# Performance work log

Measured on AMD Instinct MI355X. Metric: run time of the kernel, lower is better.

## Reference

```python
import jax, jax.numpy as jnp
import numpy as np

B, T_IN, T_OUT, V, C = 2048, 10, 25, 22, 3
D = V * C            # embed / gru hidden = 66
H = 3                # attention heads
HD = D // H          # head dim = 22
EPS = 1e-5
DIMS = [(C, 64), (64, 32), (32, 64), (64, C)]


def _bn(x, g, b):
    # eval-mode BatchNorm2d with default running stats (mean=0, var=1)
    return x * (g / jnp.sqrt(1.0 + EPS))[None, :, None, None] + b[None, :, None, None]


def _gcn_layer(x, A, Tm, cw, cb, g, bt, rw, rb, rg, rbt, pre):
    # x: (N, Cin, T, V); STSGCN ST_GCNN_layer with 1x1 conv (kernel [1,1])
    res = _bn(jnp.einsum('nctv,oc->notv', x, rw) + rb[None, :, None, None], rg, rbt)
    y = jnp.einsum('nctv,vtq->ncqv', x, Tm)   # temporal mixing
    y = jnp.einsum('nctv,tvw->nctw', y, A)    # spatial (joint) mixing
    y = _bn(jnp.einsum('nctv,oc->notv', y, cw) + cb[None, :, None, None], g, bt)
    y = y + res
    return jnp.where(y >= 0, y, pre * y)      # PReLU (scalar slope)


def setup_inputs() -> dict:
    key = jax.random.key(0)
    ks = iter(jax.random.split(key, 64))
    def rn(shape, s=0.05):
        return jax.random.normal(next(ks), shape, dtype=jnp.float32) * s
    d = {"x": rn((B, T_IN, V, C), 1.0)}
    d["A"] = rn((4, T_IN, V, V), 0.2)
    d["Tm"] = rn((4, V, T_IN, T_IN), 0.3)
    d["pre"] = jnp.full((4,), 0.25, jnp.float32)
    for i, (ci, co) in enumerate(DIMS):
        d[f"cw{i}"] = rn((co, ci), 0.1)
        d[f"cb{i}"] = rn((co,), 0.1)
        d[f"g{i}"] = jnp.ones((co,), jnp.float32)
        d[f"bt{i}"] = jnp.zeros((co,), jnp.float32)
        d[f"rw{i}"] = rn((co, ci), 0.1)
        d[f"rb{i}"] = rn((co,), 0.1)
        d[f"rg{i}"] = jnp.ones((co,), jnp.float32)
        d[f"rbt{i}"] = jnp.zeros((co,), jnp.float32)
    d["gru_wi"] = rn((3 * D, D)); d["gru_wh"] = rn((3 * D, D))
    d["gru_bi"] = rn((3 * D,));   d["gru_bh"] = rn((3 * D,))
    d["qkv_w"] = rn((3 * D, D)); d["qkv_b"] = rn((3 * D,))
    d["ow"] = rn((D, D)); d["ob"] = rn((D,))
    d["lw"] = rn((D, 2 * D)); d["lb"] = rn((D,))
    return d


def _forward(x, A, Tm, pre, cws, cbs, gs, bts, rws, rbs, rgs, rbts,
             gru_wi, gru_wh, gru_bi, gru_bh, qkv_w, qkv_b, ow, ob, lw, lb):
    raw = x.reshape(B, T_IN, D)                 # (N,T,V*C), joint-major flatten
    h = jnp.transpose(x, (0, 3, 1, 2))          # (N,C,T,V)
    for i in range(4):
        h = _gcn_layer(h, A[i], Tm[i], cws[i], cbs[i], gs[i], bts[i],
                       rws[i], rbs[i], rgs[i], rbts[i], pre[i])
    enc = jnp.transpose(h, (0, 2, 3, 1)).reshape(B, T_IN, D)  # (N,T,V*C)

    wq, wk, wv = qkv_w[:D], qkv_w[D:2 * D], qkv_w[2 * D:]
    bq, bk, bv = qkv_b[:D], qkv_b[D:2 * D], qkv_b[2 * D:]
    # K,V of encoder sequence are constant across decode steps: project once
    k = (enc @ wk.T + bk).reshape(B, T_IN, H, HD)
    v = (enc @ wv.T + bv).reshape(B, T_IN, H, HD)
    scale = 1.0 / jnp.sqrt(jnp.float32(HD))

    def gru(inp, hprev):
        gi = inp @ gru_wi.T + gru_bi
        gh = hprev @ gru_wh.T + gru_bh
        ir, iz, inn = jnp.split(gi, 3, axis=-1)
        hr, hz, hn = jnp.split(gh, 3, axis=-1)
        r = jax.nn.sigmoid(ir + hr)
        z = jax.nn.sigmoid(iz + hz)
        n = jnp.tanh(inn + r * hn)
        return (1.0 - z) * n + z * hprev

    def step(carry, _):
        hs, tp = carry
        hs = gru(tp, hs)
        q = ((hs @ wq.T + bq) * scale).reshape(B, H, HD)
        scores = jnp.einsum('bhd,bthd->bht', q, k)
        attn = jax.nn.softmax(scores, axis=-1)
        ctx = jnp.einsum('bht,bthd->bhd', attn, v).reshape(B, D) @ ow.T + ob
        pred = jnp.concatenate([hs, ctx], axis=-1) @ lw.T + lb + tp  # residual
        return (hs, pred), pred

    h0 = enc[:, -1, :]
    tp0 = raw[:, -1, :]
    _, preds = jax.lax.scan(step, (h0, tp0), None, length=T_OUT)
    out = jnp.transpose(preds, (1, 0, 2))       # (N, T_out, D)
    return out.reshape(B, T_OUT, V, C)


def reference(x, A, Tm, pre,
              cw0, cb0, g0, bt0, rw0, rb0, rg0, rbt0,
              cw1, cb1, g1, bt1, rw1, rb1, rg1, rbt1,
              cw2, cb2, g2, bt2, rw2, rb2, rg2, rbt2,
              cw3, cb3, g3, bt3, rw3, rb3, rg3, rbt3,
              gru_wi, gru_wh, gru_bi, gru_bh, qkv_w, qkv_b, ow, ob, lw, lb):
    return _forward(x, A, Tm, pre,
                    [cw0, cw1, cw2, cw3], [cb0, cb1, cb2, cb3],
                    [g0, g1, g2, g3], [bt0, bt1, bt2, bt3],
                    [rw0, rw1, rw2, rw3], [rb0, rb1, rb2, rb3],
                    [rg0, rg1, rg2, rg3], [rbt0, rbt1, rbt2, rbt3],
                    gru_wi, gru_wh, gru_bi, gru_bh, qkv_w, qkv_b, ow, ob, lw, lb)
```

## Files before the change

### kernel.cpp

```cpp
#include <hip/hip_runtime.h>

#define DEV static __device__ __forceinline__


struct EncW {
  const float* cw[4]; const float* cb[4]; const float* g[4]; const float* bt[4];
  const float* rw[4]; const float* rb[4]; const float* rg[4]; const float* rbt[4];
};

template<int CI, int CO>
DEV void gcn_layer32(int tid,
    const float* __restrict__ cw, const float* __restrict__ cb,
    const float* __restrict__ gg, const float* __restrict__ bt,
    const float* __restrict__ rw, const float* __restrict__ rb,
    const float* __restrict__ rg, const float* __restrict__ rbt,
    const float* __restrict__ TmL, const float* __restrict__ AL, float preL,
    float* __restrict__ act, float* __restrict__ S,
    float* __restrict__ rmul, float* __restrict__ radd,
    float* __restrict__ cmul, float* __restrict__ cadd)
{
  constexpr int COP8 = (CO + 7) & ~7;
  constexpr int NT = (COP8 / 8) * 55;
  const float inv = 0.99999499987f;

  for (int idx = tid; idx < CI * COP8; idx += 512) {
    int c = idx / COP8, o = idx % COP8;
    S[idx] = (o < CO) ? rw[o * CI + c] : 0.f;
  }
  for (int idx = tid; idx < 64; idx += 512) {
    bool ok = idx < CO;
    float rm = ok ? rg[idx] * inv : 0.f;
    float cm = ok ? gg[idx] * inv : 0.f;
    rmul[idx] = rm;
    radd[idx] = ok ? rb[idx] * rm + rbt[idx] : 0.f;
    cmul[idx] = cm;
    cadd[idx] = ok ? cb[idx] * cm + bt[idx] : 0.f;
  }
  __syncthreads();

  float racc[32];
  int oo = tid / 55, pp = tid % 55;
  if (tid < NT) {
    #pragma unroll
    for (int k = 0; k < 32; ++k) racc[k] = 0.f;
    #pragma unroll 4
    for (int c = 0; c < CI; ++c) {
      const float* wr = S + c * COP8 + oo * 8;
      float4 w0 = *(const float4*)(wr);
      float4 w1 = *(const float4*)(wr + 4);
      float4 av = *(const float4*)(act + c * 220 + pp * 4);
      float wv[8] = {w0.x,w0.y,w0.z,w0.w,w1.x,w1.y,w1.z,w1.w};
      #pragma unroll
      for (int o = 0; o < 8; ++o) {
        racc[o*4+0] += wv[o]*av.x; racc[o*4+1] += wv[o]*av.y;
        racc[o*4+2] += wv[o]*av.z; racc[o*4+3] += wv[o]*av.w;
      }
    }
    #pragma unroll
    for (int o = 0; o < 8; ++o) {
      float m = rmul[oo * 8 + o], a = radd[oo * 8 + o];
      #pragma unroll
      for (int k = 0; k < 4; ++k) racc[o*4+k] = racc[o*4+k]*m + a;
    }
  }
  __syncthreads();

  for (int idx = tid; idx < 2200; idx += 512) {
    int tq = idx / 22, v = idx % 22;
    int t = tq / 10, q = tq % 10;
    S[idx] = TmL[v * 100 + t * 10 + q];
  }
  __syncthreads();

  for (int idx = tid; idx < CI * 11; idx += 512) {
    int v2 = idx % 11, c = idx / 11;
    float* base = act + c * 220 + v2 * 2;
    float xin[10][2];
    #pragma unroll
    for (int t = 0; t < 10; ++t) { xin[t][0] = base[t*22]; xin[t][1] = base[t*22+1]; }
    float ya[10][2];
    #pragma unroll
    for (int q = 0; q < 10; ++q) { ya[q][0] = 0.f; ya[q][1] = 0.f; }
    #pragma unroll
    for (int t = 0; t < 10; ++t) {
      const float* tm = S + t * 220 + v2 * 2;
      #pragma unroll
      for (int q = 0; q < 10; ++q) {
        ya[q][0] += tm[q*22]   * xin[t][0];
        ya[q][1] += tm[q*22+1] * xin[t][1];
      }
    }
    #pragma unroll
    for (int q = 0; q < 10; ++q) { base[q*22] = ya[q][0]; base[q*22+1] = ya[q][1]; }
  }
  __syncthreads();

  for (int idx = tid; idx < 4840; idx += 512) S[idx] = AL[idx];
  __syncthreads();

  for (int idx = tid; idx < CI * 10; idx += 512) {
    int t = idx % 10, c = idx / 10;
    float* row = act + c * 220 + t * 22;
    float yin[22];
    #pragma unroll
    for (int v = 0; v < 22; ++v) yin[v] = row[v];
    float za[22];
    #pragma unroll
    for (int w = 0; w < 22; ++w) za[w] = 0.f;
    #pragma unroll 2
    for (int v = 0; v < 22; ++v) {
      const float* ar = S + (t * 22 + v) * 22;
      float y0 = yin[v];
      #pragma unroll
      for (int w = 0; w < 22; ++w) za[w] += y0 * ar[w];
    }
    #pragma unroll
    for (int w = 0; w < 22; ++w) row[w] = za[w];
  }
  __syncthreads();

  for (int idx = tid; idx < CI * COP8; idx += 512) {
    int c = idx / COP8, o = idx % COP8;
    S[idx] = (o < CO) ? cw[o * CI + c] : 0.f;
  }
  __syncthreads();

  float cacc[32];
  if (tid < NT) {
    #pragma unroll
    for (int k = 0; k < 32; ++k) cacc[k] = 0.f;
    #pragma unroll 4
    for (int c = 0; c < CI; ++c) {
      const float* wr = S + c * COP8 + oo * 8;
      float4 w0 = *(const float4*)(wr);
      float4 w1 = *(const float4*)(wr + 4);
      float4 av = *(const float4*)(act + c * 220 + pp * 4);
      float wv[8] = {w0.x,w0.y,w0.z,w0.w,w1.x,w1.y,w1.z,w1.w};
      #pragma unroll
      for (int o = 0; o < 8; ++o) {
        cacc[o*4+0] += wv[o]*av.x; cacc[o*4+1] += wv[o]*av.y;
        cacc[o*4+2] += wv[o]*av.z; cacc[o*4+3] += wv[o]*av.w;
      }
    }
  }
  __syncthreads();
  if (tid < NT) {
    #pragma unroll
    for (int o = 0; o < 8; ++o) {
      float m = cmul[oo * 8 + o], a = cadd[oo * 8 + o];
      #pragma unroll
      for (int k = 0; k < 4; ++k) {
        float y = cacc[o*4+k]*m + a + racc[o*4+k];
        act[(oo*8+o)*220 + pp*4 + k] = (y >= 0.f) ? y : preL * y;
      }
    }
  }
  __syncthreads();
}

__global__ __launch_bounds__(512, 4)
void enc_kernel(const float* __restrict__ x, const float* __restrict__ A,
                const float* __restrict__ Tm, const float* __restrict__ pre, EncW W,
                const float* __restrict__ qkvT, const float* __restrict__ qkv_b,
                float* __restrict__ h0_ws, float* __restrict__ k_ws,
                float* __restrict__ v_ws)
{
  __shared__ __align__(16) float act[64 * 220];
  __shared__ __align__(16) float S[4840];
  __shared__ float rmul[64], radd[64], cmul[64], cadd[64];

  const int tid = threadIdx.x;
  const int b = blockIdx.x;

  for (int idx = tid; idx < 660; idx += 512) {
    int c = idx / 220, r = idx % 220, t = r / 22, v = r % 22;
    act[c * 220 + t * 22 + v] = x[(((size_t)b * 10 + t) * 22 + v) * 3 + c];
  }
  float p0 = pre[0], p1 = pre[1], p2 = pre[2], p3 = pre[3];

  gcn_layer32<3, 64>(tid, W.cw[0], W.cb[0], W.g[0], W.bt[0], W.rw[0], W.rb[0], W.rg[0], W.rbt[0],
                     Tm, A, p0, act, S, rmul, radd, cmul, cadd);
  gcn_layer32<64, 32>(tid, W.cw[1], W.cb[1], W.g[1], W.bt[1], W.rw[1], W.rb[1], W.rg[1], W.rbt[1],
                     Tm + 2200, A + 4840, p1, act, S, rmul, radd, cmul, cadd);
  gcn_layer32<32, 64>(tid, W.cw[2], W.cb[2], W.g[2], W.bt[2], W.rw[2], W.rb[2], W.rg[2], W.rbt[2],
                     Tm + 4400, A + 9680, p2, act, S, rmul, radd, cmul, cadd);
  gcn_layer32<64, 3>(tid, W.cw[3], W.cb[3], W.g[3], W.bt[3], W.rw[3], W.rb[3], W.rg[3], W.rbt[3],
                     Tm + 6600, A + 14520, p3, act, S, rmul, radd, cmul, cadd);

  float* encD = act + 3 * 220;
  for (int idx = tid; idx < 660; idx += 512) {
    int t = idx / 66, d = idx % 66, v = d / 3, c = d % 3;
    float val = act[c * 220 + t * 22 + v];
    encD[idx] = val;
    if (t == 9) h0_ws[(size_t)b * 66 + d] = val;
  }
  __syncthreads();

  for (int idx = tid; idx < 132; idx += 512) {
    int half = idx / 66, d = idx % 66;
    int row = 66 + half * 66 + d;
    float acc[10];
    #pragma unroll
    for (int t = 0; t < 10; ++t) acc[t] = 0.f;
    for (int e = 0; e < 66; ++e) {
      float w = qkvT[e * 198 + row];
      const float* er = encD + e;
      #pragma unroll
      for (int t = 0; t < 10; ++t) acc[t] += w * er[t * 66];
    }
    float bias = qkv_b[row];
    float* dst = (half ? v_ws : k_ws) + (size_t)b * 660 + d;
    #pragma unroll
    for (int t = 0; t < 10; ++t) dst[t * 66] = acc[t] + bias;
  }
}


__global__ __launch_bounds__(512)
void prep_kernel(const float* __restrict__ qkv_w, const float* __restrict__ ow,
                 const float* __restrict__ ob, const float* __restrict__ lw,
                 const float* __restrict__ gru_wi, const float* __restrict__ gru_wh,
                 float* __restrict__ qkvT, float* __restrict__ wqD,
                 float* __restrict__ lwAT, float* __restrict__ MT,
                 float* __restrict__ cb2, float* __restrict__ wT_g)
{
  int idx = blockIdx.x * 512 + threadIdx.x;
  if (idx < 13068) {
    int e = idx / 198, j = idx % 198;
    qkvT[idx] = qkv_w[j * 66 + e];
    return;
  }
  int i1 = idx - 13068;
  if (i1 < 4356) {
    int e = i1 / 66, d = i1 % 66;
    wqD[i1] = qkv_w[d * 66 + e];
    return;
  }
  int i2 = i1 - 4356;
  if (i2 < 4356) {
    int e = i2 / 66, d = i2 % 66;
    lwAT[i2] = lw[d * 132 + e];
    return;
  }
  int i3 = i2 - 4356;
  if (i3 < 4356) {
    int e = i3 / 66, d = i3 % 66;
    const float* lrow = lw + d * 132 + 66;
    float acc = 0.f;
    for (int f = 0; f < 66; ++f) acc += lrow[f] * ow[f * 66 + e];
    MT[i3] = acc;
    return;
  }
  int i4 = i3 - 4356;
  if (i4 < 66) {
    const float* lrow = lw + i4 * 132 + 66;
    float acc = 0.f;
    for (int f = 0; f < 66; ++f) acc += lrow[f] * ob[f];
    cb2[i4] = acc;
    return;
  }
  int i5 = i4 - 66;
  if (i5 < 26136) {
    int e = i5 / 396, jm = i5 % 396;
    wT_g[i5] = (jm < 198) ? gru_wi[jm * 66 + e] : gru_wh[(jm - 198) * 66 + e];
  }
}


__global__ __launch_bounds__(512, 4)
void dec_kernel(const float* __restrict__ x, const float* __restrict__ h0_ws,
                const float* __restrict__ k_ws, const float* __restrict__ v_ws,
                const float* __restrict__ wT_g,
                const float* __restrict__ gru_bi, const float* __restrict__ gru_bh,
                const float* __restrict__ wqD, const float* __restrict__ qkv_b,
                const float* __restrict__ lwAT, const float* __restrict__ MT,
                const float* __restrict__ cb2, const float* __restrict__ lb,
                float* __restrict__ outp)
{
  __shared__ __align__(16) float wqS[4356];
  __shared__ __align__(16) float lwAS[4356];
  __shared__ __align__(16) float MS[4356];
  __shared__ __align__(16) float kS[2640];
  __shared__ __align__(16) float G[396 * 4];
  __shared__ __align__(16) float tpT[264], hsT[264], qT[264], cxT[264];
  __shared__ float attnS[120];
  __shared__ float biS[198], bhS[198], bqS[66], lbS[66];

  const int tid = threadIdx.x;
  const int b0 = blockIdx.x * 4;

  for (int idx = tid; idx < 4356; idx += 512) {
    wqS[idx] = wqD[idx]; lwAS[idx] = lwAT[idx]; MS[idx] = MT[idx];
  }
  for (int idx = tid; idx < 2640; idx += 512) {
    int r = idx / 660, rest = idx % 660;
    kS[idx] = k_ws[(size_t)(b0 + r) * 660 + rest];
  }
  for (int idx = tid; idx < 198; idx += 512) { biS[idx] = gru_bi[idx]; bhS[idx] = gru_bh[idx]; }
  for (int idx = tid; idx < 66; idx += 512)  { bqS[idx] = qkv_b[idx]; lbS[idx] = lb[idx] + cb2[idx]; }
  for (int idx = tid; idx < 264; idx += 512) {
    int d = idx >> 2, r = idx & 3;
    hsT[d * 4 + r] = h0_ws[(size_t)(b0 + r) * 66 + d];
    tpT[d * 4 + r] = x[(size_t)(b0 + r) * 660 + 594 + d];
  }
  __syncthreads();

  const float qscale = 1.0f / sqrtf(22.0f);

  for (int s = 0; s < 25; ++s) {
    if (tid < 396) {
      const float* base = (tid < 198) ? tpT : hsT;
      const float* wp = wT_g + tid;
      float a0 = 0.f, a1 = 0.f, a2 = 0.f, a3 = 0.f;
      #pragma unroll 11
      for (int e = 0; e < 66; ++e) {
        float w = wp[e * 396];
        float4 av = *(const float4*)(base + e * 4);
        a0 += w * av.x; a1 += w * av.y; a2 += w * av.z; a3 += w * av.w;
      }
      float bias = (tid < 198) ? biS[tid] : bhS[tid - 198];
      *(float4*)(G + tid * 4) = make_float4(a0 + bias, a1 + bias, a2 + bias, a3 + bias);
    }
    __syncthreads();

    if (tid < 264) {
      int d = tid >> 2, r = tid & 3;
      float ir = G[d * 4 + r]         + G[(198 + d) * 4 + r];
      float iz = G[(66 + d) * 4 + r]  + G[(264 + d) * 4 + r];
      float nx = G[(132 + d) * 4 + r];
      float hn = G[(330 + d) * 4 + r];
      float rg = 1.f / (1.f + __expf(-ir));
      float zg = 1.f / (1.f + __expf(-iz));
      float t2 = __expf(2.f * (nx + rg * hn));
      float ng = 1.f - 2.f / (t2 + 1.f);
      float h = hsT[d * 4 + r];
      hsT[d * 4 + r] = (1.f - zg) * ng + zg * h;
    }
    __syncthreads();

    if (tid < 264) {
      int r = tid / 66, d = tid % 66;
      float acc = 0.f;
      #pragma unroll 6
      for (int e = 0; e < 66; ++e)
        acc += wqS[e * 66 + d] * hsT[e * 4 + r];
      qT[d * 4 + r] = (acc + bqS[d]) * qscale;
    }
    __syncthreads();

    if (tid < 120) {
      int r = tid / 30, rem = tid % 30, h = rem / 10, t = rem % 10;
      const float* kp = kS + r * 660 + t * 66 + h * 22;
      const float* qp = qT + (h * 22) * 4 + r;
      float acc = 0.f;
      #pragma unroll
      for (int dd = 0; dd < 22; ++dd) acc += qp[dd * 4] * kp[dd];
      attnS[(r * 3 + h) * 10 + t] = acc;
    }
    __syncthreads();

    if (tid < 12) {
      float* sp = attnS + tid * 10;
      float mx = sp[0];
      #pragma unroll
      for (int t = 1; t < 10; ++t) mx = fmaxf(mx, sp[t]);
      float sum = 0.f;
      #pragma unroll
      for (int t = 0; t < 10; ++t) { float e = __expf(sp[t] - mx); sp[t] = e; sum += e; }
      float invs = 1.f / sum;
      #pragma unroll
      for (int t = 0; t < 10; ++t) sp[t] *= invs;
    }
    __syncthreads();

    if (tid < 264) {
      int r = tid / 66, d = tid % 66, h = d / 22;
      const float* ap = attnS + (r * 3 + h) * 10;
      const float* vp = v_ws + (size_t)(b0 + r) * 660 + d;
      float acc = 0.f;
      #pragma unroll
      for (int t = 0; t < 10; ++t) acc += ap[t] * vp[t * 66];
      cxT[d * 4 + r] = acc;
    }
    __syncthreads();

    if (tid < 264) {
      int r = tid / 66, d = tid % 66;
      float acc = 0.f;
      #pragma unroll 6
      for (int e = 0; e < 66; ++e)
        acc += lwAS[e * 66 + d] * hsT[e * 4 + r] + MS[e * 66 + d] * cxT[e * 4 + r];
      float pred = acc + lbS[d] + tpT[d * 4 + r];
      outp[((size_t)(b0 + r) * 25 + s) * 66 + d] = pred;
      tpT[d * 4 + r] = pred;
    }
    __syncthreads();
  }
}


extern "C" void kernel_launch(void* const* d_in, const int* in_sizes, int n_in,
                              void* d_out, int out_size, void* d_ws, size_t ws_size,
                              hipStream_t stream) {
  (void)in_sizes; (void)n_in; (void)out_size; (void)ws_size;
  const float* x   = (const float*)d_in[0];
  const float* A   = (const float*)d_in[1];
  const float* Tm  = (const float*)d_in[2];
  const float* pre = (const float*)d_in[3];
  EncW W;
  for (int i = 0; i < 4; ++i) {
    W.cw[i]  = (const float*)d_in[4 + 8 * i + 0];
    W.cb[i]  = (const float*)d_in[4 + 8 * i + 1];
    W.g[i]   = (const float*)d_in[4 + 8 * i + 2];
    W.bt[i]  = (const float*)d_in[4 + 8 * i + 3];
    W.rw[i]  = (const float*)d_in[4 + 8 * i + 4];
    W.rb[i]  = (const float*)d_in[4 + 8 * i + 5];
    W.rg[i]  = (const float*)d_in[4 + 8 * i + 6];
    W.rbt[i] = (const float*)d_in[4 + 8 * i + 7];
  }
  const float* gru_wi = (const float*)d_in[36];
  const float* gru_wh = (const float*)d_in[37];
  const float* gru_bi = (const float*)d_in[38];
  const float* gru_bh = (const float*)d_in[39];
  const float* qkv_w  = (const float*)d_in[40];
  const float* qkv_b  = (const float*)d_in[41];
  const float* ow     = (const float*)d_in[42];
  const float* ob     = (const float*)d_in[43];
  const float* lw     = (const float*)d_in[44];
  const float* lb     = (const float*)d_in[45];

  float* wsf  = (float*)d_ws;
  float* h0   = wsf;
  float* kw   = h0 + 2048 * 66;
  float* vw   = kw + 2048 * 660;
  float* qkvT = vw + 2048 * 660;
  float* wqD  = qkvT + 13068;
  float* lwAT = wqD + 4356;
  float* MT   = lwAT + 4356;
  float* cb2  = MT + 4356;
  float* wT_g = cb2 + 66;

  prep_kernel<<<103, 512, 0, stream>>>(qkv_w, ow, ob, lw, gru_wi, gru_wh,
                                       qkvT, wqD, lwAT, MT, cb2, wT_g);
  enc_kernel<<<2048, 512, 0, stream>>>(x, A, Tm, pre, W, qkvT, qkv_b, h0, kw, vw);
  dec_kernel<<<512, 512, 0, stream>>>(x, h0, kw, vw, wT_g, gru_bi, gru_bh,
                                      wqD, qkv_b, lwAT, MT, cb2, lb,
                                      (float*)d_out);
}
```

Baseline: 738.0 us.

## Restructure encoder GCN layers: direct weight reads, padded LDS, overlapped Tm staging

Rewrites the encoder GCN layer so 1x1-conv weights are read straight from global memory (float4 over channel groups) instead of being staged into shared memory, removing several staging passes and barriers per layer. The per-layer output-channel block size now varies by layer. Idle threads stage the next temporal-mixing matrix into a padded LDS layout while the residual conv runs. The adjacency matrix gets padded rows to cut bank conflicts, and shared loads and stores are vectorised. The K/V projection now uses one thread per (row, time) with padded float4 dot products over weights staged in LDS. This trades LDS staging for more global/L2 weight traffic and higher register use.

```diff
diff --git a/kernel.cpp b/kernel.cpp
--- a/kernel.cpp
+++ b/kernel.cpp
@@ -8,151 +8,180 @@
   const float* rw[4]; const float* rb[4]; const float* rg[4]; const float* rbt[4];
 };
 
-template<int CI, int CO>
-DEV void gcn_layer32(int tid,
+template<int CI, int CO, int OBLK, bool STAGE_TM>
+DEV void gcn_layer(int tid,
     const float* __restrict__ cw, const float* __restrict__ cb,
     const float* __restrict__ gg, const float* __restrict__ bt,
     const float* __restrict__ rw, const float* __restrict__ rb,
     const float* __restrict__ rg, const float* __restrict__ rbt,
     const float* __restrict__ TmL, const float* __restrict__ AL, float preL,
-    float* __restrict__ act, float* __restrict__ S,
-    float* __restrict__ rmul, float* __restrict__ radd,
-    float* __restrict__ cmul, float* __restrict__ cadd)
+    float* __restrict__ act, float* __restrict__ S)
 {
-  constexpr int COP8 = (CO + 7) & ~7;
-  constexpr int NT = (COP8 / 8) * 55;
-  const float inv = 0.99999499987f;
-
-  for (int idx = tid; idx < CI * COP8; idx += 512) {
-    int c = idx / COP8, o = idx % COP8;
-    S[idx] = (o < CO) ? rw[o * CI + c] : 0.f;
-  }
-  for (int idx = tid; idx < 64; idx += 512) {
-    bool ok = idx < CO;
-    float rm = ok ? rg[idx] * inv : 0.f;
-    float cm = ok ? gg[idx] * inv : 0.f;
-    rmul[idx] = rm;
-    radd[idx] = ok ? rb[idx] * rm + rbt[idx] : 0.f;
-    cmul[idx] = cm;
-    cadd[idx] = ok ? cb[idx] * cm + bt[idx] : 0.f;
-  }
-  __syncthreads();
-
-  float racc[32];
-  int oo = tid / 55, pp = tid % 55;
+  constexpr int NG = (CO + OBLK - 1) / OBLK;
+  constexpr int NT = NG * 55;
+  constexpr int NSPARE = 512 - NT;
+  constexpr float inv = 0.99999499987f;
+
+  const int og = tid / 55, pp = tid % 55;
+  float racc[OBLK * 4];
+
   if (tid < NT) {
-    #pragma unroll
-    for (int k = 0; k < 32; ++k) racc[k] = 0.f;
-    #pragma unroll 4
-    for (int c = 0; c < CI; ++c) {
-      const float* wr = S + c * COP8 + oo * 8;
-      float4 w0 = *(const float4*)(wr);
-      float4 w1 = *(const float4*)(wr + 4);
-      float4 av = *(const float4*)(act + c * 220 + pp * 4);
-      float wv[8] = {w0.x,w0.y,w0.z,w0.w,w1.x,w1.y,w1.z,w1.w};
-      #pragma unroll
-      for (int o = 0; o < 8; ++o) {
-        racc[o*4+0] += wv[o]*av.x; racc[o*4+1] += wv[o]*av.y;
-        racc[o*4+2] += wv[o]*av.z; racc[o*4+3] += wv[o]*av.w;
-      }
-    }
-    #pragma unroll
-    for (int o = 0; o < 8; ++o) {
-      float m = rmul[oo * 8 + o], a = radd[oo * 8 + o];
-      #pragma unroll
-      for (int k = 0; k < 4; ++k) racc[o*4+k] = racc[o*4+k]*m + a;
-    }
-  }
-  __syncthreads();
-
-  for (int idx = tid; idx < 2200; idx += 512) {
-    int tq = idx / 22, v = idx % 22;
-    int t = tq / 10, q = tq % 10;
-    S[idx] = TmL[v * 100 + t * 10 + q];
+    float bnm[OBLK], bna[OBLK];
+    #pragma unroll
+    for (int j = 0; j < OBLK; ++j) {
+      const int o = og * OBLK + j;
+      bnm[j] = rg[o] * inv;
+      bna[j] = rb[o] * bnm[j] + rbt[o];
+    }
+    #pragma unroll
+    for (int k = 0; k < OBLK * 4; ++k) racc[k] = 0.f;
+    const float* actp = act + pp * 4;
+    if constexpr (CI % 4 == 0) {
+      #pragma unroll 2
+      for (int c4 = 0; c4 < CI / 4; ++c4) {
+        float4 a0 = *(const float4*)(actp + (c4 * 4 + 0) * 220);
+        float4 a1 = *(const float4*)(actp + (c4 * 4 + 1) * 220);
+        float4 a2 = *(const float4*)(actp + (c4 * 4 + 2) * 220);
+        float4 a3 = *(const float4*)(actp + (c4 * 4 + 3) * 220);
+        #pragma unroll
+        for (int j = 0; j < OBLK; ++j) {
+          const float4 w = *(const float4*)(rw + (og * OBLK + j) * CI + c4 * 4);
+          racc[j*4+0] += w.x*a0.x + w.y*a1.x + w.z*a2.x + w.w*a3.x;
+          racc[j*4+1] += w.x*a0.y + w.y*a1.y + w.z*a2.y + w.w*a3.y;
+          racc[j*4+2] += w.x*a0.z + w.y*a1.z + w.z*a2.z + w.w*a3.z;
+          racc[j*4+3] += w.x*a0.w + w.y*a1.w + w.z*a2.w + w.w*a3.w;
+        }
+      }
+    } else {
+      #pragma unroll
+      for (int c = 0; c < CI; ++c) {
+        float4 av = *(const float4*)(actp + c * 220);
+        #pragma unroll
+        for (int j = 0; j < OBLK; ++j) {
+          const float w = rw[(og * OBLK + j) * CI + c];
+          racc[j*4+0] += w * av.x; racc[j*4+1] += w * av.y;
+          racc[j*4+2] += w * av.z; racc[j*4+3] += w * av.w;
+        }
+      }
+    }
+    #pragma unroll
+    for (int j = 0; j < OBLK; ++j) {
+      #pragma unroll
+      for (int k = 0; k < 4; ++k) racc[j*4+k] = racc[j*4+k] * bnm[j] + bna[j];
+    }
+  } else if constexpr (STAGE_TM) {
+    for (int i = tid - NT; i < 2200; i += NSPARE) {
+      const int v = i / 100, r = i % 100;
+      S[(r / 10) * 264 + v * 12 + (r % 10)] = TmL[i];
+    }
   }
   __syncthreads();
 
   for (int idx = tid; idx < CI * 11; idx += 512) {
-    int v2 = idx % 11, c = idx / 11;
+    const int v2 = idx % 11, c = idx / 11;
     float* base = act + c * 220 + v2 * 2;
-    float xin[10][2];
-    #pragma unroll
-    for (int t = 0; t < 10; ++t) { xin[t][0] = base[t*22]; xin[t][1] = base[t*22+1]; }
-    float ya[10][2];
-    #pragma unroll
-    for (int q = 0; q < 10; ++q) { ya[q][0] = 0.f; ya[q][1] = 0.f; }
+    float x0[10], x1[10];
     #pragma unroll
     for (int t = 0; t < 10; ++t) {
-      const float* tm = S + t * 220 + v2 * 2;
+      float2 xv = *(const float2*)(base + t * 22);
+      x0[t] = xv.x; x1[t] = xv.y;
+    }
+    float y0[10], y1[10];
+    #pragma unroll
+    for (int q = 0; q < 10; ++q) { y0[q] = 0.f; y1[q] = 0.f; }
+    #pragma unroll
+    for (int t = 0; t < 10; ++t) {
+      const float* tm = S + t * 264 + v2 * 24;
       #pragma unroll
       for (int q = 0; q < 10; ++q) {
-        ya[q][0] += tm[q*22]   * xin[t][0];
-        ya[q][1] += tm[q*22+1] * xin[t][1];
-      }
-    }
-    #pragma unroll
-    for (int q = 0; q < 10; ++q) { base[q*22] = ya[q][0]; base[q*22+1] = ya[q][1]; }
-  }
-  __syncthreads();
-
-  for (int idx = tid; idx < 4840; idx += 512) S[idx] = AL[idx];
+        y0[q] += tm[q]      * x0[t];
+        y1[q] += tm[q + 12] * x1[t];
+      }
+    }
+    #pragma unroll
+    for (int q = 0; q < 10; ++q)
+      *(float2*)(base + q * 22) = make_float2(y0[q], y1[q]);
+  }
+  __syncthreads();
+
+  for (int i = tid; i < 4840; i += 512) {
+    const int r = i / 22, w = i - r * 22;
+    S[r * 28 + w] = AL[i];
+  }
   __syncthreads();
 
   for (int idx = tid; idx < CI * 10; idx += 512) {
-    int t = idx % 10, c = idx / 10;
+    const int t = idx % 10, c = idx / 10;
     float* row = act + c * 220 + t * 22;
     float yin[22];
     #pragma unroll
-    for (int v = 0; v < 22; ++v) yin[v] = row[v];
+    for (int v2 = 0; v2 < 11; ++v2) {
+      float2 y = *(const float2*)(row + 2 * v2);
+      yin[2*v2] = y.x; yin[2*v2+1] = y.y;
+    }
     float za[22];
     #pragma unroll
     for (int w = 0; w < 22; ++w) za[w] = 0.f;
     #pragma unroll 2
     for (int v = 0; v < 22; ++v) {
-      const float* ar = S + (t * 22 + v) * 22;
-      float y0 = yin[v];
-      #pragma unroll
-      for (int w = 0; w < 22; ++w) za[w] += y0 * ar[w];
-    }
-    #pragma unroll
-    for (int w = 0; w < 22; ++w) row[w] = za[w];
-  }
-  __syncthreads();
-
-  for (int idx = tid; idx < CI * COP8; idx += 512) {
-    int c = idx / COP8, o = idx % COP8;
-    S[idx] = (o < CO) ? cw[o * CI + c] : 0.f;
-  }
-  __syncthreads();
-
-  float cacc[32];
+      const float* ar = S + (t * 22 + v) * 28;
+      const float y0v = yin[v];
+      #pragma unroll
+      for (int w = 0; w < 22; ++w) za[w] += y0v * ar[w];
+    }
+    #pragma unroll
+    for (int v2 = 0; v2 < 11; ++v2)
+      *(float2*)(row + 2 * v2) = make_float2(za[2*v2], za[2*v2+1]);
+  }
+  __syncthreads();
+
+  float cacc[OBLK * 4];
   if (tid < NT) {
     #pragma unroll
-    for (int k = 0; k < 32; ++k) cacc[k] = 0.f;
-    #pragma unroll 4
-    for (int c = 0; c < CI; ++c) {
-      const float* wr = S + c * COP8 + oo * 8;
-      float4 w0 = *(const float4*)(wr);
-      float4 w1 = *(const float4*)(wr + 4);
-      float4 av = *(const float4*)(act + c * 220 + pp * 4);
-      float wv[8] = {w0.x,w0.y,w0.z,w0.w,w1.x,w1.y,w1.z,w1.w};
-      #pragma unroll
-      for (int o = 0; o < 8; ++o) {
-        cacc[o*4+0] += wv[o]*av.x; cacc[o*4+1] += wv[o]*av.y;
-        cacc[o*4+2] += wv[o]*av.z; cacc[o*4+3] += wv[o]*av.w;
+    for (int k = 0; k < OBLK * 4; ++k) cacc[k] = 0.f;
+    const float* actp = act + pp * 4;
+    if constexpr (CI % 4 == 0) {
+      #pragma unroll 2
+      for (int c4 = 0; c4 < CI / 4; ++c4) {
+        float4 a0 = *(const float4*)(actp + (c4 * 4 + 0) * 220);
+        float4 a1 = *(const float4*)(actp + (c4 * 4 + 1) * 220);
+        float4 a2 = *(const float4*)(actp + (c4 * 4 + 2) * 220);
+        float4 a3 = *(const float4*)(actp + (c4 * 4 + 3) * 220);
+        #pragma unroll
+        for (int j = 0; j < OBLK; ++j) {
+          const float4 w = *(const float4*)(cw + (og * OBLK + j) * CI + c4 * 4);
+          cacc[j*4+0] += w.x*a0.x + w.y*a1.x + w.z*a2.x + w.w*a3.x;
+          cacc[j*4+1] += w.x*a0.y + w.y*a1.y + w.z*a2.y + w.w*a3.y;
+          cacc[j*4+2] += w.x*a0.z + w.y*a1.z + w.z*a2.z + w.w*a3.z;
+          cacc[j*4+3] += w.x*a0.w + w.y*a1.w + w.z*a2.w + w.w*a3.w;
+        }
+      }
+    } else {
+      #pragma unroll
+      for (int c = 0; c < CI; ++c) {
+        float4 av = *(const float4*)(actp + c * 220);
+        #pragma unroll
+        for (int j = 0; j < OBLK; ++j) {
+          const float w = cw[(og * OBLK + j) * CI + c];
+          cacc[j*4+0] += w * av.x; cacc[j*4+1] += w * av.y;
+          cacc[j*4+2] += w * av.z; cacc[j*4+3] += w * av.w;
+        }
       }
     }
   }
   __syncthreads();
   if (tid < NT) {
     #pragma unroll
-    for (int o = 0; o < 8; ++o) {
-      float m = cmul[oo * 8 + o], a = cadd[oo * 8 + o];
-      #pragma unroll
-      for (int k = 0; k < 4; ++k) {
-        float y = cacc[o*4+k]*m + a + racc[o*4+k];
-        act[(oo*8+o)*220 + pp*4 + k] = (y >= 0.f) ? y : preL * y;
-      }
+    for (int j = 0; j < OBLK; ++j) {
+      const int o = og * OBLK + j;
+      const float m = gg[o] * inv;
+      const float a = cb[o] * m + bt[o];
+      float4 out; float y;
+      y = cacc[j*4+0]*m + a + racc[j*4+0]; out.x = (y >= 0.f) ? y : preL * y;
+      y = cacc[j*4+1]*m + a + racc[j*4+1]; out.y = (y >= 0.f) ? y : preL * y;
+      y = cacc[j*4+2]*m + a + racc[j*4+2]; out.z = (y >= 0.f) ? y : preL * y;
+      y = cacc[j*4+3]*m + a + racc[j*4+3]; out.w = (y >= 0.f) ? y : preL * y;
+      *(float4*)(act + o * 220 + pp * 4) = out;
     }
   }
   __syncthreads();
@@ -161,57 +190,75 @@
 __global__ __launch_bounds__(512, 4)
 void enc_kernel(const float* __restrict__ x, const float* __restrict__ A,
                 const float* __restrict__ Tm, const float* __restrict__ pre, EncW W,
-                const float* __restrict__ qkvT, const float* __restrict__ qkv_b,
+                const float* __restrict__ qkv_w, const float* __restrict__ qkv_b,
                 float* __restrict__ h0_ws, float* __restrict__ k_ws,
                 float* __restrict__ v_ws)
 {
   __shared__ __align__(16) float act[64 * 220];
-  __shared__ __align__(16) float S[4840];
-  __shared__ float rmul[64], radd[64], cmul[64], cadd[64];
+  __shared__ __align__(16) float S[220 * 28];
 
   const int tid = threadIdx.x;
   const int b = blockIdx.x;
-
-  for (int idx = tid; idx < 660; idx += 512) {
-    int c = idx / 220, r = idx % 220, t = r / 22, v = r % 22;
-    act[c * 220 + t * 22 + v] = x[(((size_t)b * 10 + t) * 22 + v) * 3 + c];
-  }
-  float p0 = pre[0], p1 = pre[1], p2 = pre[2], p3 = pre[3];
-
-  gcn_layer32<3, 64>(tid, W.cw[0], W.cb[0], W.g[0], W.bt[0], W.rw[0], W.rb[0], W.rg[0], W.rbt[0],
-                     Tm, A, p0, act, S, rmul, radd, cmul, cadd);
-  gcn_layer32<64, 32>(tid, W.cw[1], W.cb[1], W.g[1], W.bt[1], W.rw[1], W.rb[1], W.rg[1], W.rbt[1],
-                     Tm + 2200, A + 4840, p1, act, S, rmul, radd, cmul, cadd);
-  gcn_layer32<32, 64>(tid, W.cw[2], W.cb[2], W.g[2], W.bt[2], W.rw[2], W.rb[2], W.rg[2], W.rbt[2],
-                     Tm + 4400, A + 9680, p2, act, S, rmul, radd, cmul, cadd);
-  gcn_layer32<64, 3>(tid, W.cw[3], W.cb[3], W.g[3], W.bt[3], W.rw[3], W.rb[3], W.rg[3], W.rbt[3],
-                     Tm + 6600, A + 14520, p3, act, S, rmul, radd, cmul, cadd);
-
-  float* encD = act + 3 * 220;
-  for (int idx = tid; idx < 660; idx += 512) {
-    int t = idx / 66, d = idx % 66, v = d / 3, c = d % 3;
-    float val = act[c * 220 + t * 22 + v];
-    encD[idx] = val;
-    if (t == 9) h0_ws[(size_t)b * 66 + d] = val;
-  }
-  __syncthreads();
-
-  for (int idx = tid; idx < 132; idx += 512) {
-    int half = idx / 66, d = idx % 66;
-    int row = 66 + half * 66 + d;
-    float acc[10];
-    #pragma unroll
-    for (int t = 0; t < 10; ++t) acc[t] = 0.f;
-    for (int e = 0; e < 66; ++e) {
-      float w = qkvT[e * 198 + row];
-      const float* er = encD + e;
-      #pragma unroll
-      for (int t = 0; t < 10; ++t) acc[t] += w * er[t * 66];
-    }
-    float bias = qkv_b[row];
-    float* dst = (half ? v_ws : k_ws) + (size_t)b * 660 + d;
-    #pragma unroll
-    for (int t = 0; t < 10; ++t) dst[t * 66] = acc[t] + bias;
+  const float* xb = x + (size_t)b * 660;
+
+  for (int i = tid; i < 165; i += 512) {
+    float4 xv = *(const float4*)(xb + i * 4);
+    const int f = i * 4;
+    act[((f    ) % 3) * 220 + (f    ) / 3] = xv.x;
+    act[((f + 1) % 3) * 220 + (f + 1) / 3] = xv.y;
+    act[((f + 2) % 3) * 220 + (f + 2) / 3] = xv.z;
+    act[((f + 3) % 3) * 220 + (f + 3) / 3] = xv.w;
+  }
+  for (int i = tid; i < 2200; i += 512) {
+    const int v = i / 100, r = i % 100;
+    S[(r / 10) * 264 + v * 12 + (r % 10)] = Tm[i];
+  }
+  const float p0 = pre[0], p1 = pre[1], p2 = pre[2], p3 = pre[3];
+  __syncthreads();
+
+  gcn_layer<3, 64, 8, false>(tid, W.cw[0], W.cb[0], W.g[0], W.bt[0], W.rw[0], W.rb[0], W.rg[0], W.rbt[0],
+                             Tm, A, p0, act, S);
+  gcn_layer<64, 32, 4, true>(tid, W.cw[1], W.cb[1], W.g[1], W.bt[1], W.rw[1], W.rb[1], W.rg[1], W.rbt[1],
+                             Tm + 2200, A + 4840, p1, act, S);
+  gcn_layer<32, 64, 8, true>(tid, W.cw[2], W.cb[2], W.g[2], W.bt[2], W.rw[2], W.rb[2], W.rg[2], W.rbt[2],
+                             Tm + 4400, A + 9680, p2, act, S);
+  gcn_layer<64, 3, 1, true>(tid, W.cw[3], W.cb[3], W.g[3], W.bt[3], W.rw[3], W.rb[3], W.rg[3], W.rbt[3],
+                             Tm + 6600, A + 14520, p3, act, S);
+
+  float* encD = act + 660;
+  float* wKVS = act + 1344;
+  for (int i = tid; i < 680; i += 512) {
+    const int t = i / 68, d = i % 68;
+    float val = 0.f;
+    if (d < 66) {
+      const int v = d / 3, c = d % 3;
+      val = act[c * 220 + t * 22 + v];
+      if (t == 9) h0_ws[(size_t)b * 66 + d] = val;
+    }
+    encD[i] = val;
+  }
+  for (int i = tid; i < 132 * 68; i += 512) {
+    const int r = i / 68, e = i % 68;
+    float vv = 0.f;
+    if (e < 66) vv = qkv_w[4356 + r * 66 + e];
+    wKVS[i] = vv;
+  }
+  __syncthreads();
+
+  for (int idx = tid; idx < 1320; idx += 512) {
+    const int row = idx / 10, t = idx % 10;
+    const float4* wp = (const float4*)(wKVS + row * 68);
+    const float4* ep = (const float4*)(encD + t * 68);
+    float acc = 0.f;
+    #pragma unroll
+    for (int j = 0; j < 17; ++j) {
+      const float4 w = wp[j], e = ep[j];
+      acc += w.x * e.x + w.y * e.y + w.z * e.z + w.w * e.w;
+    }
+    acc += qkv_b[66 + row];
+    const int d = (row < 66) ? row : row - 66;
+    float* dst = (row < 66) ? k_ws : v_ws;
+    dst[(size_t)b * 660 + t * 66 + d] = acc;
   }
 }
 
@@ -442,7 +489,7 @@
 
   prep_kernel<<<103, 512, 0, stream>>>(qkv_w, ow, ob, lw, gru_wi, gru_wh,
                                        qkvT, wqD, lwAT, MT, cb2, wT_g);
-  enc_kernel<<<2048, 512, 0, stream>>>(x, A, Tm, pre, W, qkvT, qkv_b, h0, kw, vw);
+  enc_kernel<<<2048, 512, 0, stream>>>(x, A, Tm, pre, W, qkv_w, qkv_b, h0, kw, vw);
   dec_kernel<<<512, 512, 0, stream>>>(x, h0, kw, vw, wT_g, gru_bi, gru_bh,
                                       wqD, qkv_b, lwAT, MT, cb2, lb,
                                       (float*)d_out);
```

Result: slower. 863.7 us (+17.0%).
